# Kernel tuning notes

Hardware: AMD Instinct MI355X
Metric: run time of the kernel (lower is better)

## Reference

```python
import jax, jax.numpy as jnp
import numpy as np

WINDOW = 11
C1 = 0.01 ** 2
C2 = 0.03 ** 2
PAD = WINDOW // 2


def _box_filter(img, kernel):
    # img: [B,1,H,W], kernel: [1,1,w,w]; SAME padding (odd window)
    return jax.lax.conv_general_dilated(
        img, kernel,
        window_strides=(1, 1),
        padding=[(PAD, PAD), (PAD, PAD)],
        dimension_numbers=('NCHW', 'OIHW', 'NCHW'))


def setup_inputs() -> dict:
    key = jax.random.key(0)
    kx, ky = jax.random.split(key)
    B, C, H, W = 64, 1, 512, 512
    x = jax.random.uniform(kx, (B, C, H, W), dtype=jnp.float32)
    y = jax.random.uniform(ky, (B, C, H, W), dtype=jnp.float32)
    kernel = jnp.ones((1, 1, WINDOW, WINDOW), dtype=jnp.float32) / (WINDOW ** 2)
    return {"x": x, "y": y, "kernel": kernel}


def reference(x, y, kernel):
    mu_x = _box_filter(x, kernel)
    mu_y = _box_filter(y, kernel)
    mu_x2 = mu_x * mu_x
    mu_y2 = mu_y * mu_y
    mu_xy = mu_x * mu_y
    sigma_x2 = _box_filter(x * x, kernel) - mu_x2
    sigma_y2 = _box_filter(y * y, kernel) - mu_y2
    sigma_xy = _box_filter(x * y, kernel) - mu_xy
    ssim_map = ((2.0 * mu_xy + C1) * (2.0 * sigma_xy + C2)) / (
        (mu_x2 + mu_y2 + C1) * (sigma_x2 + sigma_y2 + C2))
    return 1.0 - jnp.mean(ssim_map)
```

## Files before the change

### kernel.cpp

```cpp
#include <hip/hip_runtime.h>
#include <stdint.h>


#define IMG_H 512
#define IMG_W 512
#define N_IMG 64
#define RAD   5
#define SH    64
#define NBANDG 8
#define NBLOCKS (N_IMG * NBANDG)
#define NSLOT 13

#define C1_SSIM 1.0e-4f
#define C2_SSIM 9.0e-4f

#define SLOT_BYTES 4096

typedef __attribute__((address_space(3))) uint32_t lds_u32_t;
typedef const __attribute__((address_space(1))) uint32_t glb_u32_t;

__device__ __forceinline__ void dma16(void* lds, const void* g) {
    __builtin_amdgcn_global_load_lds((glb_u32_t*)g, (lds_u32_t*)lds, 16, 0, 0);
}

__global__ __launch_bounds__(64) void ssim_fused(const float* __restrict__ x,
                                                 const float* __restrict__ y,
                                                 float* __restrict__ part)
{
    __shared__ __align__(16) char ring[NSLOT][SLOT_BYTES];

    const int tx  = threadIdx.x;

    const int wid = (blockIdx.x & 7) * (NBLOCKS / 8) + (blockIdx.x >> 3);
    const int img = wid >> 3;
    const int bg  = wid & (NBANDG - 1);
    const int r0  = bg * SH;

    const float* __restrict__ xi = x + (size_t)img * (IMG_H * IMG_W);
    const float* __restrict__ yi = y + (size_t)img * (IMG_H * IMG_W);

    auto dma_row = [&](int slot, int ri) {
        int rc = ri < 0 ? 0 : (ri > IMG_H - 1 ? IMG_H - 1 : ri);
        char* s = &ring[slot][0];
        const char* xg = (const char*)(xi + (size_t)rc * IMG_W) + tx * 16;
        const char* yg = (const char*)(yi + (size_t)rc * IMG_W) + tx * 16;
        dma16(s,        xg);
        dma16(s + 1024, xg + 1024);
        dma16(s + 2048, yg);
        dma16(s + 3072, yg + 1024);
    };

    float Vx[8], Vy[8], Vss[8], Vxy[8];
#pragma unroll
    for (int j = 0; j < 8; ++j) { Vx[j] = 0.f; Vy[j] = 0.f; Vss[j] = 0.f; Vxy[j] = 0.f; }

    auto accum_add = [&](const char* s, float f) {
        const float4* xr = (const float4*)(s + (size_t)tx * 32);
        const float4* yr = (const float4*)(s + 2048 + (size_t)tx * 32);
        float4 x0 = xr[0], x1 = xr[1];
        float4 y0 = yr[0], y1 = yr[1];
        float xs[8] = {x0.x, x0.y, x0.z, x0.w, x1.x, x1.y, x1.z, x1.w};
        float ys[8] = {y0.x, y0.y, y0.z, y0.w, y1.x, y1.y, y1.z, y1.w};
#pragma unroll
        for (int j = 0; j < 8; ++j) {
            float fx = f * xs[j];
            float fy = f * ys[j];
            Vx[j] += fx;
            Vy[j] += fy;
            Vss[j] = fmaf(fx, xs[j], Vss[j]);
            Vss[j] = fmaf(fy, ys[j], Vss[j]);
            Vxy[j] = fmaf(fx, ys[j], Vxy[j]);
        }
    };

    auto accum_sub = [&](const char* s) {
        const float4* xr = (const float4*)(s + (size_t)tx * 32);
        const float4* yr = (const float4*)(s + 2048 + (size_t)tx * 32);
        float4 x0 = xr[0], x1 = xr[1];
        float4 y0 = yr[0], y1 = yr[1];
        float xs[8] = {x0.x, x0.y, x0.z, x0.w, x1.x, x1.y, x1.z, x1.w};
        float ys[8] = {y0.x, y0.y, y0.z, y0.w, y1.x, y1.y, y1.z, y1.w};
#pragma unroll
        for (int j = 0; j < 8; ++j) {
            Vx[j]  -= xs[j];
            Vy[j]  -= ys[j];
            Vss[j] = fmaf(-xs[j], xs[j], Vss[j]);
            Vss[j] = fmaf(-ys[j], ys[j], Vss[j]);
            Vxy[j] = fmaf(-xs[j], ys[j], Vxy[j]);
        }
    };

    auto hsum = [&](const float (&V)[8], float (&S)[8]) {
        float w[18];
#pragma unroll
        for (int k = 0; k < 5; ++k) {
            float l = __shfl_up(V[3 + k], 1, 64);
            w[k] = (tx == 0) ? 0.f : l;
        }
#pragma unroll
        for (int j = 0; j < 8; ++j) w[5 + j] = V[j];
#pragma unroll
        for (int k = 0; k < 5; ++k) {
            float r = __shfl_down(V[k], 1, 64);
            w[13 + k] = (tx == 63) ? 0.f : r;
        }
        float s = 0.f;
#pragma unroll
        for (int t = 0; t < 11; ++t) s += w[t];
        S[0] = s;
#pragma unroll
        for (int j = 1; j < 8; ++j) { s += w[j + 10] - w[j - 1]; S[j] = s; }
    };

#pragma unroll 1
    for (int i = 0; i < 11; ++i) dma_row(i, r0 - RAD + i);
#pragma unroll 1
    for (int i = 0; i < 10; ++i) {
        int ri = r0 - RAD + i;
        accum_add(&ring[i][0], ri >= 0 ? 1.0f : 0.0f);
    }

    const float inv121 = 1.0f / 121.0f;
    float loss = 0.0f;
    int sAdd = 10, sSub = 12, sPre = 11;
    const int subLo = (r0 > 0) ? (r0 - RAD) : 0;

#pragma unroll 1
    for (int r = r0; r < r0 + SH; ++r) {
        accum_add(&ring[sAdd][0], (r + RAD < IMG_H) ? 1.0f : 0.0f);

        int rs = r - RAD - 1;
        if (rs >= subLo) accum_sub(&ring[sSub][0]);

        if (r < r0 + SH - 1) dma_row(sPre, r + RAD + 1);

        float Sx[8], Sy[8], Sss[8], Sxy[8];
        hsum(Vx,  Sx);
        hsum(Vy,  Sy);
        hsum(Vss, Sss);
        hsum(Vxy, Sxy);

#pragma unroll
        for (int j = 0; j < 8; ++j) {
            float mx  = Sx[j] * inv121;
            float my  = Sy[j] * inv121;
            float mx2 = mx * mx;
            float my2 = my * my;
            float mxy = mx * my;
            float vs  = Sss[j] * inv121 - mx2 - my2;
            float vxy = Sxy[j] * inv121 - mxy;
            float num = (2.0f * mxy + C1_SSIM) * (2.0f * vxy + C2_SSIM);
            float den = (mx2 + my2 + C1_SSIM) * (vs + C2_SSIM);
            loss += __fdividef(num, den);
        }

        if (++sAdd == NSLOT) sAdd = 0;
        if (++sSub == NSLOT) sSub = 0;
        if (++sPre == NSLOT) sPre = 0;
    }

#pragma unroll
    for (int off = 32; off > 0; off >>= 1)
        loss += __shfl_down(loss, off, 64);
    if (tx == 0)
        part[blockIdx.x] = loss;
}

__global__ __launch_bounds__(256) void ssim_reduce(const float* __restrict__ part,
                                                   float* __restrict__ out)
{
    const int t  = threadIdx.x;
    const int tx = t & 63;
    float s = part[t] + part[t + 256];
#pragma unroll
    for (int off = 32; off > 0; off >>= 1)
        s += __shfl_down(s, off, 64);
    __shared__ float ws[4];
    if (tx == 0) ws[t >> 6] = s;
    __syncthreads();
    if (t == 0) {
        float total = (ws[0] + ws[1]) + (ws[2] + ws[3]);
        out[0] = 1.0f - total * (1.0f / ((float)N_IMG * IMG_H * IMG_W));
    }
}

extern "C" void kernel_launch(void* const* d_in, const int* in_sizes, int n_in,
                              void* d_out, int out_size, void* d_ws, size_t ws_size,
                              hipStream_t stream) {
    const float* x = (const float*)d_in[0];
    const float* y = (const float*)d_in[1];
    float* part = (float*)d_ws;

    ssim_fused<<<NBLOCKS, 64, 0, stream>>>(x, y, part);
    ssim_reduce<<<1, 256, 0, stream>>>(part, (float*)d_out);
}
```

Baseline: 192.6 us.

## Split each row band across two waves sharing an LDS ring, simplify SSIM arithmetic

Each block now runs two wavefronts that interleave output rows (even/odd) over the same band. They share a 16-slot LDS ring of DMA'd rows, synchronised with __syncthreads, and each wave slides its vertical window by two rows per step. The SSIM formula is rewritten on unnormalised sums with pre-scaled constants to remove the per-pixel divisions by 121. This doubles threads per block and adds latency hiding, at the cost of a block barrier every iteration and twice the vertical add/sub work per output row.

```diff
diff --git a/kernel.cpp b/kernel.cpp
--- a/kernel.cpp
+++ b/kernel.cpp
@@ -6,13 +6,13 @@
 #define IMG_W 512
 #define N_IMG 64
 #define RAD   5
-#define SH    64
+#define BAND  64
 #define NBANDG 8
 #define NBLOCKS (N_IMG * NBANDG)
-#define NSLOT 13
-
-#define C1_SSIM 1.0e-4f
-#define C2_SSIM 9.0e-4f
+#define NSLOT 16
+
+#define C1S2 1.4641f
+#define C2S2 13.1769f
 
 #define SLOT_BYTES 4096
 
@@ -23,18 +23,20 @@
     __builtin_amdgcn_global_load_lds((glb_u32_t*)g, (lds_u32_t*)lds, 16, 0, 0);
 }
 
-__global__ __launch_bounds__(64) void ssim_fused(const float* __restrict__ x,
-                                                 const float* __restrict__ y,
-                                                 float* __restrict__ part)
+__global__ __launch_bounds__(128) void ssim_fused(const float* __restrict__ x,
+                                                  const float* __restrict__ y,
+                                                  float* __restrict__ part)
 {
     __shared__ __align__(16) char ring[NSLOT][SLOT_BYTES];
 
-    const int tx  = threadIdx.x;
+    const int tx = threadIdx.x & 63;
+    const int wv = threadIdx.x >> 6;
 
     const int wid = (blockIdx.x & 7) * (NBLOCKS / 8) + (blockIdx.x >> 3);
     const int img = wid >> 3;
     const int bg  = wid & (NBANDG - 1);
-    const int r0  = bg * SH;
+    const int r0  = bg * BAND;
+    const int q0  = r0 + wv;
 
     const float* __restrict__ xi = x + (size_t)img * (IMG_H * IMG_W);
     const float* __restrict__ yi = y + (size_t)img * (IMG_H * IMG_W);
@@ -113,26 +115,30 @@
     };
 
 #pragma unroll 1
-    for (int i = 0; i < 11; ++i) dma_row(i, r0 - RAD + i);
+    for (int k = wv; k < 14; k += 2) dma_row(k, r0 - 7 + k);
+    __syncthreads();
 #pragma unroll 1
-    for (int i = 0; i < 10; ++i) {
-        int ri = r0 - RAD + i;
-        accum_add(&ring[i][0], ri >= 0 ? 1.0f : 0.0f);
+    for (int t = 0; t < 11; ++t) {
+        int row = q0 - 7 + t;
+        accum_add(&ring[wv + t][0], row >= 0 ? 1.0f : 0.0f);
     }
 
-    const float inv121 = 1.0f / 121.0f;
     float loss = 0.0f;
-    int sAdd = 10, sSub = 12, sPre = 11;
-    const int subLo = (r0 > 0) ? (r0 - RAD) : 0;
+    int sa = wv + 11;
+    int ss = wv;
+    int sp = wv + 14;
 
 #pragma unroll 1
-    for (int r = r0; r < r0 + SH; ++r) {
-        accum_add(&ring[sAdd][0], (r + RAD < IMG_H) ? 1.0f : 0.0f);
-
-        int rs = r - RAD - 1;
-        if (rs >= subLo) accum_sub(&ring[sSub][0]);
-
-        if (r < r0 + SH - 1) dma_row(sPre, r + RAD + 1);
+    for (int i = 0; i < BAND / 2; ++i) {
+        const int q = q0 + 2 * i;
+
+        accum_add(&ring[sa][0],            (q + 4 < IMG_H) ? 1.0f : 0.0f);
+        accum_add(&ring[(sa + 1) & 15][0], (q + 5 < IMG_H) ? 1.0f : 0.0f);
+
+        if (q - 7 >= 0) accum_sub(&ring[ss][0]);
+        if (q - 6 >= 0) accum_sub(&ring[(ss + 1) & 15][0]);
+
+        if (i < BAND / 2 - 1) dma_row(sp & 15, q + 7);
 
         float Sx[8], Sy[8], Sss[8], Sxy[8];
         hsum(Vx,  Sx);
@@ -142,28 +148,31 @@
 
 #pragma unroll
         for (int j = 0; j < 8; ++j) {
-            float mx  = Sx[j] * inv121;
-            float my  = Sy[j] * inv121;
-            float mx2 = mx * mx;
-            float my2 = my * my;
-            float mxy = mx * my;
-            float vs  = Sss[j] * inv121 - mx2 - my2;
-            float vxy = Sxy[j] * inv121 - mxy;
-            float num = (2.0f * mxy + C1_SSIM) * (2.0f * vxy + C2_SSIM);
-            float den = (mx2 + my2 + C1_SSIM) * (vs + C2_SSIM);
-            loss += __fdividef(num, den);
-        }
-
-        if (++sAdd == NSLOT) sAdd = 0;
-        if (++sSub == NSLOT) sSub = 0;
-        if (++sPre == NSLOT) sPre = 0;
+            float A  = Sx[j] * Sy[j];
+            float B  = fmaf(Sx[j], Sx[j], Sy[j] * Sy[j]);
+            float n1 = fmaf(A, 2.0f, C1S2);
+            float n2 = fmaf(Sxy[j], 242.0f, fmaf(A, -2.0f, C2S2));
+            float d1 = B + C1S2;
+            float d2 = fmaf(Sss[j], 121.0f, C2S2 - B);
+            loss += __fdividef(n1 * n2, d1 * d2);
+        }
+
+        sa = (sa + 2) & 15;
+        ss = (ss + 2) & 15;
+        sp = (sp + 2) & 15;
+
+        __syncthreads();
     }
 
 #pragma unroll
     for (int off = 32; off > 0; off >>= 1)
         loss += __shfl_down(loss, off, 64);
-    if (tx == 0)
-        part[blockIdx.x] = loss;
+
+    float* pr = reinterpret_cast<float*>(&ring[0][0]);
+    if (tx == 0) pr[wv] = loss;
+    __syncthreads();
+    if (threadIdx.x == 0)
+        part[blockIdx.x] = pr[0] + pr[1];
 }
 
 __global__ __launch_bounds__(256) void ssim_reduce(const float* __restrict__ part,
@@ -191,6 +200,6 @@
     const float* y = (const float*)d_in[1];
     float* part = (float*)d_ws;
 
-    ssim_fused<<<NBLOCKS, 64, 0, stream>>>(x, y, part);
+    ssim_fused<<<NBLOCKS, 128, 0, stream>>>(x, y, part);
     ssim_reduce<<<1, 256, 0, stream>>>(part, (float*)d_out);
 }
```

Result: faster. 166.4 us (-13.6%).
